# Performance work log

Hardware: AMD Instinct MI355X
Metric: run time of the kernel (lower is better)

## Reference

```python
import jax, jax.numpy as jnp
import numpy as np

DIM = 1024
N_HEADS = 16
MLP_DIM = 4096
DEPTH = 6
HEAD_DIM = DIM // N_HEADS
SCALE = DIM ** -0.5  # module uses full dim (self.dim_heads = dim), NOT head_dim
EPS = 1e-5


def setup_inputs() -> dict:
    key = jax.random.key(0)
    ks = jax.random.split(key, 12)
    s = lambda k, shape, fan: jax.random.normal(k, shape, jnp.float32) * (fan ** -0.5)
    return {
        "x": jax.random.normal(ks[0], (8, 1024, DIM), jnp.float32),
        "Wq": s(ks[1], (DIM, DIM), DIM), "bq": jnp.zeros((DIM,), jnp.float32),
        "Wk": s(ks[2], (DIM, DIM), DIM), "bk": jnp.zeros((DIM,), jnp.float32),
        "Wv": s(ks[3], (DIM, DIM), DIM), "bv": jnp.zeros((DIM,), jnp.float32),
        "W1": s(ks[4], (DIM, MLP_DIM), DIM), "b1": jnp.zeros((MLP_DIM,), jnp.float32),
        "W2": s(ks[5], (MLP_DIM, DIM), MLP_DIM), "b2": jnp.zeros((DIM,), jnp.float32),
        "gamma": jnp.ones((DIM,), jnp.float32),
        "beta": jnp.zeros((DIM,), jnp.float32),
    }


def _layernorm(x, gamma, beta):
    mu = jnp.mean(x, axis=-1, keepdims=True)
    var = jnp.mean(jnp.square(x - mu), axis=-1, keepdims=True)
    return (x - mu) * jax.lax.rsqrt(var + EPS) * gamma + beta


def _attention(x, Wq, bq, Wk, bk, Wv, bv):
    b, n, _ = x.shape
    split = lambda t: t.reshape(b, n, N_HEADS, HEAD_DIM).transpose(0, 2, 1, 3)  # b h n d
    q = split(x @ Wq + bq)
    k = split(x @ Wk + bk)
    v = split(x @ Wv + bv)
    logit = jnp.einsum('bhnd,bhmd->bhnm', q, k) * SCALE
    attn = jax.nn.softmax(logit, axis=-1)
    out = jnp.einsum('bhnm,bhmd->bhnd', attn, v)
    return out.transpose(0, 2, 1, 3).reshape(b, n, DIM)


def reference(x, Wq, bq, Wk, bk, Wv, bv, W1, b1, W2, b2, gamma, beta):
    # Same single attention + MLP modules (shared weights) applied `depth` times.
    for _ in range(DEPTH):
        x = _attention(_layernorm(x, gamma, beta), Wq, bq, Wk, bk, Wv, bv) + x
        h = _layernorm(x, gamma, beta)
        x = (jax.nn.gelu(h @ W1 + b1, approximate=False) @ W2 + b2) + x
    return x
```

## Files before the change

kernel.cpp:

```cpp
#include <hip/hip_runtime.h>
#include <cstdint>
#include <cmath>

typedef short bf16x8 __attribute__((ext_vector_type(8)));
typedef float f32x4 __attribute__((ext_vector_type(4)));

#define AS_GLOBAL(p) (const __attribute__((address_space(1))) void*)(p)
#define AS_LDS(p)    (__attribute__((address_space(3))) void*)(p)

#define QSCALE 0.04508422002778f

__device__ inline float b2f(unsigned short u) {
    union { unsigned int i; float f; } c; c.i = ((unsigned int)u) << 16; return c.f;
}
__device__ inline unsigned short f2b(float f) {
    return (unsigned short)((__float_as_uint(f) + 0x8000u) >> 16);
}
__device__ inline uint2 pk4(float a, float b, float c, float d) {
    unsigned ua = __float_as_uint(a) + 0x8000u;
    unsigned ub = __float_as_uint(b) + 0x8000u;
    unsigned uc = __float_as_uint(c) + 0x8000u;
    unsigned ud = __float_as_uint(d) + 0x8000u;
    uint2 r;
    r.x = (ua >> 16) | (ub & 0xffff0000u);
    r.y = (uc >> 16) | (ud & 0xffff0000u);
    return r;
}
__device__ inline unsigned cvt_pk_bf16u(float lo, float hi) {
    unsigned r;
    asm("v_cvt_pk_bf16_f32 %0, %1, %2" : "=v"(r) : "v"(lo), "v"(hi));
    return r;
}
__device__ inline float fast_gelu(float x) {
    float arg = -x * (2.30223674f + 0.10294946f * x * x);
    float t = exp2f(arg);
    return x * __builtin_amdgcn_rcpf(1.f + t);
}

__device__ inline bf16x8 ldsfrag(const unsigned short* SM, int base_sh, int r, int lc) {
    return *(const bf16x8*)((const char*)SM + base_sh * 2 + r * 128 + ((lc ^ (r & 7)) << 4));
}

__global__ __launch_bounds__(256) void transpose_f32_to_bf16(
    const float* __restrict__ W, unsigned short* __restrict__ Wt, int K, int N)
{
    __shared__ unsigned short sh[32][33];
    int n0 = blockIdx.x * 32;
    int k0 = blockIdx.y * 32;
    int tr = threadIdx.x >> 5;
    int tc = threadIdx.x & 31;
#pragma unroll
    for (int i = 0; i < 4; i++)
        sh[tr + i * 8][tc] = f2b(W[(size_t)(k0 + tr + i * 8) * N + n0 + tc]);
    __syncthreads();
#pragma unroll
    for (int i = 0; i < 4; i++)
        Wt[(size_t)(n0 + tr + i * 8) * K + k0 + tc] = sh[tc][tr + i * 8];
}

__global__ __launch_bounds__(256) void concat_bias(const float* __restrict__ bq,
                                                   const float* __restrict__ bk,
                                                   float* __restrict__ bqk)
{
    int i = blockIdx.x * 256 + threadIdx.x;
    bqk[i] = (i < 1024) ? bq[i] : bk[i - 1024];
}

__global__ __launch_bounds__(256) void copy_f32(const float* __restrict__ in,
                                                float* __restrict__ out)
{
    size_t i = ((size_t)blockIdx.x * 256 + threadIdx.x) * 8;
    f32x4 a = *(const f32x4*)(in + i);
    f32x4 b = *(const f32x4*)(in + i + 4);
    *(f32x4*)(out + i) = a;
    *(f32x4*)(out + i + 4) = b;
}

__global__ __launch_bounds__(256) void layernorm_k(
    const float* __restrict__ x, const float* __restrict__ gamma,
    const float* __restrict__ beta, unsigned short* __restrict__ out)
{
    int row = blockIdx.x;
    int t = threadIdx.x;
    f32x4 v = *(const f32x4*)(x + (size_t)row * 1024 + t * 4);
    float s  = v[0] + v[1] + v[2] + v[3];
    float s2 = v[0]*v[0] + v[1]*v[1] + v[2]*v[2] + v[3]*v[3];
#pragma unroll
    for (int off = 32; off >= 1; off >>= 1) {
        s  += __shfl_xor(s,  off);
        s2 += __shfl_xor(s2, off);
    }
    __shared__ float red[8];
    int w = t >> 6;
    if ((t & 63) == 0) { red[w] = s; red[4 + w] = s2; }
    __syncthreads();
    s  = red[0] + red[1] + red[2] + red[3];
    s2 = red[4] + red[5] + red[6] + red[7];
    float mu  = s * (1.f / 1024.f);
    float var = s2 * (1.f / 1024.f) - mu * mu;
    float rs  = rsqrtf(var + 1e-5f);
    int c = t * 4;
    f32x4 g = *(const f32x4*)(gamma + c);
    f32x4 be = *(const f32x4*)(beta + c);
    unsigned int lo, hi;
    {
        float o0 = (v[0] - mu) * rs * g[0] + be[0];
        float o1 = (v[1] - mu) * rs * g[1] + be[1];
        float o2 = (v[2] - mu) * rs * g[2] + be[2];
        float o3 = (v[3] - mu) * rs * g[3] + be[3];
        lo = (unsigned)f2b(o0) | ((unsigned)f2b(o1) << 16);
        hi = (unsigned)f2b(o2) | ((unsigned)f2b(o3) << 16);
    }
    uint2 pk; pk.x = lo; pk.y = hi;
    *(uint2*)(out + (size_t)row * 1024 + c) = pk;
}

template<int MODE, int NBXL>
__global__ __launch_bounds__(256) void gemm_bt(
    const unsigned short* __restrict__ A,
    const unsigned short* __restrict__ Bt,
    const float* __restrict__ bias,
    void* __restrict__ outp,
    int M, int N, int K)
{
    __shared__ unsigned short As[128 * 32];
    __shared__ unsigned short Bs[128 * 32];
    const int t = threadIdx.x;

    const int bi   = blockIdx.x;
    const int xcd  = bi & 7;
    const int j    = bi >> 3;
    const int nby8 = M >> 10;
    const int m_idx = xcd * nby8 + (j >> NBXL);
    const int n_idx = j & ((1 << NBXL) - 1);
    const int n0 = n_idx * 128;
    const int m0 = m_idx * 128;

    const int lane = t & 63;
    const int wave = t >> 6;
    const int wm = (wave >> 1) * 64;
    const int wn = (wave & 1) * 64;
    const int lm = lane & 15;
    const int q  = lane >> 4;

    const int pos0 = wave * 128 + lane;
    const int row0 = pos0 >> 2;
    const int row1 = (pos0 + 64) >> 2;
    const int cg0  = (pos0 & 3) << 3;
    const int ldsb = wave * 1024;

    f32x4 acc[4][4];
#pragma unroll
    for (int i = 0; i < 4; i++)
#pragma unroll
        for (int n = 0; n < 4; n++) acc[i][n] = (f32x4)0.f;

    for (int k0 = 0; k0 < K; k0 += 32) {
        __syncthreads();
        {
            const unsigned short* ga0 = A  + (size_t)(m0 + row0) * K + k0 + cg0;
            const unsigned short* ga1 = A  + (size_t)(m0 + row1) * K + k0 + cg0;
            const unsigned short* gb0 = Bt + (size_t)(n0 + row0) * K + k0 + cg0;
            const unsigned short* gb1 = Bt + (size_t)(n0 + row1) * K + k0 + cg0;
            __builtin_amdgcn_global_load_lds(AS_GLOBAL(ga0), AS_LDS(As + ldsb),       16, 0, 0);
            __builtin_amdgcn_global_load_lds(AS_GLOBAL(ga1), AS_LDS(As + ldsb + 512), 16, 0, 0);
            __builtin_amdgcn_global_load_lds(AS_GLOBAL(gb0), AS_LDS(Bs + ldsb),       16, 0, 0);
            __builtin_amdgcn_global_load_lds(AS_GLOBAL(gb1), AS_LDS(Bs + ldsb + 512), 16, 0, 0);
        }
        __syncthreads();
        bf16x8 af[4], bfr[4];
#pragma unroll
        for (int i = 0; i < 4; i++)
            af[i] = *(const bf16x8*)(As + (wm + i * 16 + lm) * 32 + q * 8);
#pragma unroll
        for (int n = 0; n < 4; n++)
            bfr[n] = *(const bf16x8*)(Bs + (wn + n * 16 + lm) * 32 + q * 8);
#pragma unroll
        for (int i = 0; i < 4; i++)
#pragma unroll
            for (int n = 0; n < 4; n++)
                acc[i][n] = __builtin_amdgcn_mfma_f32_16x16x32_bf16(af[i], bfr[n], acc[i][n], 0, 0, 0);
    }

#pragma unroll
    for (int i = 0; i < 4; i++) {
#pragma unroll
        for (int n = 0; n < 4; n++) {
            int gc = n0 + wn + n * 16 + lm;
#pragma unroll
            for (int r = 0; r < 4; r++) {
                int gr = m0 + wm + i * 16 + q * 4 + r;
                float v = acc[i][n][r] + bias[gr];
                ((unsigned short*)outp)[(size_t)gr * N + gc] = f2b(v);
            }
        }
    }
}

template<int MODE, int NBNL, int BN>
__global__ __launch_bounds__(512, 2) void gemm256(
    const unsigned short* __restrict__ A,
    const unsigned short* __restrict__ Bt,
    const float* __restrict__ bias,
    void* __restrict__ outp,
    int M, int N, int K)
{
    constexpr int NFR = BN / 64;
    constexpr int WGN = BN / 64;
    constexpr int WM  = 2 * WGN;
    extern __shared__ unsigned short LDS[];

    const int t   = threadIdx.x;
    const int bi  = blockIdx.x;
    const int xcd = bi & 7;
    const int j   = bi >> 3;
    const int mper = M >> 11;
    const int m0 = (xcd * mper + (j >> NBNL)) * 256;
    const int n0 = (j & ((1 << NBNL) - 1)) * BN;

    const int w    = t >> 6;
    const int lane = t & 63;
    const int l15  = lane & 15;
    const int q    = lane >> 4;
    const int wmb  = (w / WGN) * (WM * 16);
    const int wnb  = (w % WGN) * 64;
    const int xsw  = (l15 & 7) << 4;

    const int trow = t >> 3;
    const int csrc = ((t & 7) ^ (trow & 7)) << 3;
    const unsigned short* As0 = A  + (size_t)(m0 + trow) * K + csrc;
    const unsigned short* Bs0 = Bt + (size_t)(n0 + trow) * K + csrc;

    f32x4 acc[WM][4];
#pragma unroll
    for (int i = 0; i < WM; i++)
#pragma unroll
        for (int n = 0; n < 4; n++) acc[i][n] = (f32x4)0.f;

    auto STAGE = [&](int Tn) {
        const int bsel = Tn & 1;
        const size_t kk = (size_t)Tn << 6;
#pragma unroll
        for (int la = 0; la < 4; la++)
            __builtin_amdgcn_global_load_lds(
                AS_GLOBAL(As0 + (size_t)la * 64 * K + kk),
                AS_LDS(LDS + bsel * 16384 + la * 4096 + w * 512), 16, 0, 0);
#pragma unroll
        for (int lb = 0; lb < NFR; lb++)
            __builtin_amdgcn_global_load_lds(
                AS_GLOBAL(Bs0 + (size_t)lb * 64 * K + kk),
                AS_LDS(LDS + 32768 + bsel * (BN * 64) + lb * 4096 + w * 512), 16, 0, 0);
    };

    STAGE(0);
    asm volatile("s_waitcnt vmcnt(0)" ::: "memory");
    __builtin_amdgcn_s_barrier();

    const int NT = K >> 6;
    for (int T = 0; T < NT; T++) {
        if (T + 1 < NT) STAGE(T + 1);
        const char* Ab = (const char*)LDS + (T & 1) * 32768;
        const char* Bb = (const char*)LDS + 65536 + (T & 1) * (BN * 128);
#pragma unroll
        for (int ks = 0; ks < 2; ks++) {
            const int colx = ((ks * 64 + q * 16) ^ xsw);
            bf16x8 bfv[4];
#pragma unroll
            for (int ni = 0; ni < 4; ni++)
                bfv[ni] = *(const bf16x8*)(Bb + (wnb + ni * 16 + l15) * 128 + colx);
#pragma unroll
            for (int mh = 0; mh < 2; mh++) {
                bf16x8 af[WM / 2];
#pragma unroll
                for (int m4 = 0; m4 < WM / 2; m4++)
                    af[m4] = *(const bf16x8*)(Ab + (wmb + (mh * (WM / 2) + m4) * 16 + l15) * 128 + colx);
                __builtin_amdgcn_s_setprio(1);
#pragma unroll
                for (int m4 = 0; m4 < WM / 2; m4++)
#pragma unroll
                    for (int ni = 0; ni < 4; ni++)
                        acc[mh * (WM / 2) + m4][ni] = __builtin_amdgcn_mfma_f32_16x16x32_bf16(
                            af[m4], bfv[ni], acc[mh * (WM / 2) + m4][ni], 0, 0, 0);
                __builtin_amdgcn_s_setprio(0);
                __builtin_amdgcn_sched_barrier(0);
                if (!(ks == 1 && mh == 1)) __builtin_amdgcn_s_barrier();
            }
        }
        asm volatile("s_waitcnt vmcnt(0)" ::: "memory");
        __builtin_amdgcn_s_barrier();
    }

    const float qsc = (MODE == 5 && n0 < 1024) ? QSCALE : 1.f;
#pragma unroll
    for (int mi = 0; mi < WM; mi++) {
        const int gr0 = m0 + wmb + mi * 16 + q * 4;
#pragma unroll
        for (int ni = 0; ni < 4; ni++) {
            const int gc = n0 + wnb + ni * 16 + l15;
            const float bv = bias[gc];
#pragma unroll
            for (int r = 0; r < 4; r++) {
                const int gr = gr0 + r;
                float v = acc[mi][ni][r] + bv;
                if (MODE == 1) {
                    ((unsigned short*)outp)[(size_t)gr * N + gc] = f2b(fast_gelu(v));
                } else if (MODE == 2) {
                    ((float*)outp)[(size_t)gr * N + gc] += v;
                } else {
                    ((unsigned short*)outp)[(size_t)gr * N + gc] = f2b(v * qsc);
                }
            }
        }
    }
}

__global__ __launch_bounds__(256, 4) void attn_k(
    const unsigned short* __restrict__ qkb,
    const unsigned short* __restrict__ vtb,
    float* __restrict__ x)
{
    __shared__ unsigned short SM[20480];

    const int t    = threadIdx.x;
    const int blk  = blockIdx.x;
    const int qt   = blk & 7;
    const int h    = (blk >> 3) & 15;
    const int b    = blk >> 7;
    const int w    = t >> 6;
    const int lane = t & 63;
    const int l15  = lane & 15;
    const int quad = lane >> 4;
    const int wrow = w * 32;

    const int sr  = t >> 3;
    const int slc = (t & 7) ^ (sr & 7);
    const unsigned short* Qsrc = qkb + ((size_t)(b * 1024 + qt * 128 + sr)) * 2048 + h * 64 + slc * 8;
    const unsigned short* Ksrc = qkb + ((size_t)(b * 1024 + sr)) * 2048 + 1024 + h * 64 + slc * 8;
    const unsigned short* Vsrc = vtb + ((size_t)(h * 64 + sr)) * 8192 + (size_t)b * 1024 + slc * 8;

    auto GLL = [&](const unsigned short* g, int sh) {
        __builtin_amdgcn_global_load_lds(AS_GLOBAL(g), AS_LDS(SM + sh + w * 512), 16, 0, 0);
    };

#pragma unroll
    for (int c = 0; c < 4; c++) GLL(Qsrc + (size_t)c * 32 * 2048, c * 2048);
#pragma unroll
    for (int c = 0; c < 2; c++) GLL(Ksrc + (size_t)c * 32 * 2048, 8192 + c * 2048);
#pragma unroll
    for (int c = 0; c < 2; c++) GLL(Ksrc + (size_t)(64 + c * 32) * 2048, 12288 + c * 2048);
#pragma unroll
    for (int c = 0; c < 2; c++) GLL(Vsrc + (size_t)c * 32 * 8192, 16384 + c * 2048);
    asm volatile("s_waitcnt vmcnt(0)" ::: "memory");
    __builtin_amdgcn_s_barrier();

    bf16x8 qf[2][2];
#pragma unroll
    for (int nt2 = 0; nt2 < 2; nt2++)
#pragma unroll
        for (int kd = 0; kd < 2; kd++)
            qf[nt2][kd] = ldsfrag(SM, 0, wrow + nt2 * 16 + l15, kd * 4 + quad);

    const bf16x8 onesv = (bf16x8)(short)0x3F80;
    float m_s[2] = { -1e30f, -1e30f };
    f32x4 l_acc[2] = { (f32x4)0.f, (f32x4)0.f };
    f32x4 O[2][4];
#pragma unroll
    for (int nt2 = 0; nt2 < 2; nt2++)
#pragma unroll
        for (int dt = 0; dt < 4; dt++) O[nt2][dt] = (f32x4)0.f;

    for (int kt = 0; kt < 16; ++kt) {
        const int cur = kt & 1;
        if (kt > 0) {
            const unsigned short* vs = Vsrc + kt * 64;
            GLL(vs, 16384);
            GLL(vs + (size_t)32 * 8192, 16384 + 2048);
        }

        f32x4 s[4][2];
#pragma unroll
        for (int mt = 0; mt < 4; mt++) {
            bf16x8 kf0 = ldsfrag(SM, 8192 + cur * 4096, mt * 16 + l15, quad);
            bf16x8 kf1 = ldsfrag(SM, 8192 + cur * 4096, mt * 16 + l15, 4 + quad);
#pragma unroll
            for (int nt2 = 0; nt2 < 2; nt2++) {
                f32x4 a = (f32x4)0.f;
                a = __builtin_amdgcn_mfma_f32_16x16x32_bf16(kf0, qf[nt2][0], a, 0, 0, 0);
                a = __builtin_amdgcn_mfma_f32_16x16x32_bf16(kf1, qf[nt2][1], a, 0, 0, 0);
                s[mt][nt2] = a;
            }
        }

#pragma unroll
        for (int nt2 = 0; nt2 < 2; nt2++) {
            float tm = -1e30f;
#pragma unroll
            for (int mt = 0; mt < 4; mt++) {
                f32x4 sv = s[mt][nt2];
                tm = fmaxf(tm, fmaxf(fmaxf(sv[0], sv[1]), fmaxf(sv[2], sv[3])));
            }
            tm = fmaxf(tm, __shfl_xor(tm, 16));
            tm = fmaxf(tm, __shfl_xor(tm, 32));
            if (!__all(tm <= m_s[nt2])) {
                float nm    = fmaxf(m_s[nt2], tm);
                float alpha = exp2f(m_s[nt2] - nm);
                m_s[nt2] = nm;
                l_acc[nt2] *= alpha;
#pragma unroll
                for (int dt = 0; dt < 4; dt++) O[nt2][dt] *= alpha;
            }
            const float nm = m_s[nt2];
            const int r = wrow + nt2 * 16 + l15;
#pragma unroll
            for (int mt = 0; mt < 4; mt++) {
                float p0 = exp2f(s[mt][nt2][0] - nm);
                float p1 = exp2f(s[mt][nt2][1] - nm);
                float p2 = exp2f(s[mt][nt2][2] - nm);
                float p3 = exp2f(s[mt][nt2][3] - nm);
                uint2 pk;
                pk.x = cvt_pk_bf16u(p0, p1);
                pk.y = cvt_pk_bf16u(p2, p3);
                *(uint2*)((char*)SM + r * 128 + (((2 * mt + (quad >> 1)) ^ (r & 7)) << 4)
                          + (quad & 1) * 8) = pk;
            }
        }

        asm volatile("s_waitcnt vmcnt(0)" ::: "memory");
        __builtin_amdgcn_s_barrier();

        if (kt + 2 < 16) {
            const unsigned short* ks = Ksrc + (size_t)(kt + 2) * 64 * 2048;
            GLL(ks, 8192 + cur * 4096);
            GLL(ks + (size_t)32 * 2048, 8192 + cur * 4096 + 2048);
        }

        bf16x8 pf[2][2];
#pragma unroll
        for (int nt2 = 0; nt2 < 2; nt2++)
#pragma unroll
            for (int kc = 0; kc < 2; kc++)
                pf[nt2][kc] = ldsfrag(SM, 0, wrow + nt2 * 16 + l15, kc * 4 + quad);
#pragma unroll
        for (int nt2 = 0; nt2 < 2; nt2++) {
            l_acc[nt2] = __builtin_amdgcn_mfma_f32_16x16x32_bf16(onesv, pf[nt2][0], l_acc[nt2], 0, 0, 0);
            l_acc[nt2] = __builtin_amdgcn_mfma_f32_16x16x32_bf16(onesv, pf[nt2][1], l_acc[nt2], 0, 0, 0);
        }
#pragma unroll
        for (int dt = 0; dt < 4; dt++) {
            bf16x8 vf0 = ldsfrag(SM, 16384, dt * 16 + l15, quad);
            bf16x8 vf1 = ldsfrag(SM, 16384, dt * 16 + l15, 4 + quad);
#pragma unroll
            for (int nt2 = 0; nt2 < 2; nt2++) {
                O[nt2][dt] = __builtin_amdgcn_mfma_f32_16x16x32_bf16(vf0, pf[nt2][0], O[nt2][dt], 0, 0, 0);
                O[nt2][dt] = __builtin_amdgcn_mfma_f32_16x16x32_bf16(vf1, pf[nt2][1], O[nt2][dt], 0, 0, 0);
            }
        }

        __builtin_amdgcn_s_barrier();
    }

    {
        float inv0 = 1.f / l_acc[0][0], inv1 = 1.f / l_acc[1][0];
#pragma unroll
        for (int nt2 = 0; nt2 < 2; nt2++) {
            float inv = (nt2 == 0) ? inv0 : inv1;
            const int r = wrow + nt2 * 16 + l15;
#pragma unroll
            for (int dt = 0; dt < 4; dt++) {
                uint2 pk;
                pk.x = cvt_pk_bf16u(O[nt2][dt][0] * inv, O[nt2][dt][1] * inv);
                pk.y = cvt_pk_bf16u(O[nt2][dt][2] * inv, O[nt2][dt][3] * inv);
                *(uint2*)((char*)SM + 16384 + r * 128 + (((2 * dt + (quad >> 1)) ^ (r & 7)) << 4)
                          + (quad & 1) * 8) = pk;
            }
        }
    }
    __syncthreads();
    {
        int r0 = t >> 2;
        int qc = t & 3;
#pragma unroll
        for (int half = 0; half < 2; half++) {
            int r = r0 + half * 64;
            float* xp = x + ((size_t)(b * 1024 + qt * 128 + r)) * 1024 + h * 64 + qc * 16;
#pragma unroll
            for (int jj = 0; jj < 2; jj++) {
                uint4 u = *(const uint4*)((const char*)SM + 16384 + r * 128
                                          + (((qc * 2 + jj) ^ (r & 7)) << 4));
                f32x4 xv0 = *(f32x4*)(xp + jj * 8);
                f32x4 xv1 = *(f32x4*)(xp + jj * 8 + 4);
                xv0[0] += b2f((unsigned short)(u.x & 0xffff));
                xv0[1] += b2f((unsigned short)(u.x >> 16));
                xv0[2] += b2f((unsigned short)(u.y & 0xffff));
                xv0[3] += b2f((unsigned short)(u.y >> 16));
                xv1[0] += b2f((unsigned short)(u.z & 0xffff));
                xv1[1] += b2f((unsigned short)(u.z >> 16));
                xv1[2] += b2f((unsigned short)(u.w & 0xffff));
                xv1[3] += b2f((unsigned short)(u.w >> 16));
                *(f32x4*)(xp + jj * 8)     = xv0;
                *(f32x4*)(xp + jj * 8 + 4) = xv1;
            }
        }
    }
}

extern "C" void kernel_launch(void* const* d_in, const int* in_sizes, int n_in,
                              void* d_out, int out_size, void* d_ws, size_t ws_size,
                              hipStream_t stream)
{
    (void)in_sizes; (void)n_in; (void)out_size; (void)ws_size;
    const float* x_in  = (const float*)d_in[0];
    const float* Wq    = (const float*)d_in[1];
    const float* bq    = (const float*)d_in[2];
    const float* Wk    = (const float*)d_in[3];
    const float* bk    = (const float*)d_in[4];
    const float* Wv    = (const float*)d_in[5];
    const float* bv    = (const float*)d_in[6];
    const float* W1    = (const float*)d_in[7];
    const float* b1    = (const float*)d_in[8];
    const float* W2    = (const float*)d_in[9];
    const float* b2    = (const float*)d_in[10];
    const float* gamma = (const float*)d_in[11];
    const float* beta  = (const float*)d_in[12];

    char* base = (char*)d_ws;
    float*          xf   = (float*)(base);
    unsigned short* xn   = (unsigned short*)(base + 33554432);
    unsigned short* qkb  = (unsigned short*)(base + 50331648);
    unsigned short* vtb  = (unsigned short*)(base + 50331648 + 33554432);
    unsigned short* h1   = (unsigned short*)(base + 50331648);
    char* wbase = base + 50331648 + 67108864;
    unsigned short* WqkT = (unsigned short*)(wbase);
    unsigned short* WvT  = (unsigned short*)(wbase + 4194304);
    unsigned short* W1T  = (unsigned short*)(wbase + 6291456);
    unsigned short* W2T  = (unsigned short*)(wbase + 14680064);
    float*          bqk  = (float*)(wbase + 23068672);

    transpose_f32_to_bf16<<<dim3(32, 32),  256, 0, stream>>>(Wq, WqkT, 1024, 1024);
    transpose_f32_to_bf16<<<dim3(32, 32),  256, 0, stream>>>(Wk, WqkT + 1048576, 1024, 1024);
    transpose_f32_to_bf16<<<dim3(32, 32),  256, 0, stream>>>(Wv, WvT, 1024, 1024);
    transpose_f32_to_bf16<<<dim3(128, 32), 256, 0, stream>>>(W1, W1T, 1024, 4096);
    transpose_f32_to_bf16<<<dim3(32, 128), 256, 0, stream>>>(W2, W2T, 4096, 1024);
    concat_bias<<<8, 256, 0, stream>>>(bq, bk, bqk);
    copy_f32<<<4096, 256, 0, stream>>>(x_in, xf);

    for (int layer = 0; layer < 6; ++layer) {
        layernorm_k<<<8192, 256, 0, stream>>>(xf, gamma, beta, xn);
        gemm256<5, 3, 256><<<256, 512, 131072, stream>>>(xn, WqkT, bqk, qkb, 8192, 2048, 1024);
        gemm_bt<3, 6><<<512, 256, 0, stream>>>(WvT, xn, bv, vtb, 1024, 8192, 1024);
        attn_k<<<1024, 256, 0, stream>>>(qkb, vtb, xf);
        layernorm_k<<<8192, 256, 0, stream>>>(xf, gamma, beta, xn);
        gemm256<1, 4, 256><<<512, 512, 131072, stream>>>(xn, W1T, b1, h1, 8192, 4096, 1024);
        gemm256<2, 3, 128><<<256, 512, 98304, stream>>>(h1, W2T, b2, xf, 8192, 1024, 4096);
    }
    copy_f32<<<4096, 256, 0, stream>>>(xf, (float*)d_out);
}
```

Measured before the change: 2.020 ms.

## Split K across warp groups inside W2 GEMM tile with LDS reduction

```diff
diff --git a/kernel.cpp b/kernel.cpp
--- a/kernel.cpp
+++ b/kernel.cpp
@@ -15,16 +15,6 @@
 }
 __device__ inline unsigned short f2b(float f) {
     return (unsigned short)((__float_as_uint(f) + 0x8000u) >> 16);
-}
-__device__ inline uint2 pk4(float a, float b, float c, float d) {
-    unsigned ua = __float_as_uint(a) + 0x8000u;
-    unsigned ub = __float_as_uint(b) + 0x8000u;
-    unsigned uc = __float_as_uint(c) + 0x8000u;
-    unsigned ud = __float_as_uint(d) + 0x8000u;
-    uint2 r;
-    r.x = (ua >> 16) | (ub & 0xffff0000u);
-    r.y = (uc >> 16) | (ud & 0xffff0000u);
-    return r;
 }
 __device__ inline unsigned cvt_pk_bf16u(float lo, float hi) {
     unsigned r;
@@ -197,7 +187,7 @@
     }
 }
 
-template<int MODE, int NBNL, int BN>
+template<int MODE, int NBNL, int BN, int KSPLIT = 1>
 __global__ __launch_bounds__(512, 2) void gemm256(
     const unsigned short* __restrict__ A,
     const unsigned short* __restrict__ Bt,
@@ -207,7 +197,8 @@
 {
     constexpr int NFR = BN / 64;
     constexpr int WGN = BN / 64;
-    constexpr int WM  = 2 * WGN;
+    constexpr int WM  = (KSPLIT == 2) ? 8 : 2 * WGN;
+    constexpr int KSI = (KSPLIT == 2) ? 1 : 2;
     extern __shared__ unsigned short LDS[];
 
     const int t   = threadIdx.x;
@@ -222,8 +213,9 @@
     const int lane = t & 63;
     const int l15  = lane & 15;
     const int q    = lane >> 4;
-    const int wmb  = (w / WGN) * (WM * 16);
-    const int wnb  = (w % WGN) * 64;
+    const int wmb  = (KSPLIT == 2) ? ((w >> 1) & 1) * 128 : (w / WGN) * (WM * 16);
+    const int wnb  = (KSPLIT == 2) ? (w & 1) * 64        : (w % WGN) * 64;
+    const int ksw  = (KSPLIT == 2) ? (w >> 2) : 0;
     const int xsw  = (l15 & 7) << 4;
 
     const int trow = t >> 3;
@@ -262,7 +254,8 @@
         const char* Ab = (const char*)LDS + (T & 1) * 32768;
         const char* Bb = (const char*)LDS + 65536 + (T & 1) * (BN * 128);
 #pragma unroll
-        for (int ks = 0; ks < 2; ks++) {
+        for (int ksi = 0; ksi < KSI; ksi++) {
+            const int ks = (KSPLIT == 2) ? ksw : ksi;
             const int colx = ((ks * 64 + q * 16) ^ xsw);
             bf16x8 bfv[4];
 #pragma unroll
@@ -283,11 +276,38 @@
                             af[m4], bfv[ni], acc[mh * (WM / 2) + m4][ni], 0, 0, 0);
                 __builtin_amdgcn_s_setprio(0);
                 __builtin_amdgcn_sched_barrier(0);
-                if (!(ks == 1 && mh == 1)) __builtin_amdgcn_s_barrier();
+                if (!(ksi == KSI - 1 && mh == 1)) __builtin_amdgcn_s_barrier();
             }
         }
         asm volatile("s_waitcnt vmcnt(0)" ::: "memory");
         __builtin_amdgcn_s_barrier();
+    }
+
+    if (KSPLIT == 2) {
+        float* red = (float*)LDS;
+        const int p = w & 3;
+#pragma unroll
+        for (int chunk = 0; chunk < 2; chunk++) {
+            __syncthreads();
+            if (ksw == 1) {
+#pragma unroll
+                for (int mi = 0; mi < 4; mi++)
+#pragma unroll
+                    for (int ni = 0; ni < 4; ni++)
+                        *(f32x4*)(red + p * 4096 + ((mi * 4 + ni) * 64 + lane) * 4)
+                            = acc[chunk * 4 + mi][ni];
+            }
+            __syncthreads();
+            if (ksw == 0) {
+#pragma unroll
+                for (int mi = 0; mi < 4; mi++)
+#pragma unroll
+                    for (int ni = 0; ni < 4; ni++)
+                        acc[chunk * 4 + mi][ni] +=
+                            *(const f32x4*)(red + p * 4096 + ((mi * 4 + ni) * 64 + lane) * 4);
+            }
+        }
+        if (ksw == 1) return;
     }
 
     const float qsc = (MODE == 5 && n0 < 1024) ? QSCALE : 1.f;
@@ -551,7 +571,7 @@
         attn_k<<<1024, 256, 0, stream>>>(qkb, vtb, xf);
         layernorm_k<<<8192, 256, 0, stream>>>(xf, gamma, beta, xn);
         gemm256<1, 4, 256><<<512, 512, 131072, stream>>>(xn, W1T, b1, h1, 8192, 4096, 1024);
-        gemm256<2, 3, 128><<<256, 512, 98304, stream>>>(h1, W2T, b2, xf, 8192, 1024, 4096);
+        gemm256<2, 3, 128, 2><<<256, 512, 98304, stream>>>(h1, W2T, b2, xf, 8192, 1024, 4096);
     }
     copy_f32<<<4096, 256, 0, stream>>>(xf, (float*)d_out);
 }
```

After: 2.037 ms. Within noise of the previous version (+0.9%).
